# Kernel tuning notes

Hardware: AMD Instinct MI355X
Metric: run time of the kernel (lower is better)

Reference implementation:

```python
import jax, jax.numpy as jnp
import numpy as np

EPS = 1e-6  # torch F.pairwise_distance default eps added to the difference


def setup_inputs() -> dict:
    key = jax.random.key(0)
    k1, k2 = jax.random.split(key)
    x = jax.random.normal(k1, (8, 4096, 512), dtype=jnp.float32)
    centroids = jax.random.normal(k2, (2048, 512), dtype=jnp.float32)
    return {"x": x, "centroids": centroids}


def reference(x, centroids):
    # Faithful to KMeans.forward with normalize=None, p_norm=2, return_centroids=True.
    # torch pairwise_distance computes ||x - c + eps||_2; expand algebraically with
    # xe = x + eps to avoid materializing the (b, k, d) broadcast:
    #   ||xe - c||^2 = ||xe||^2 - 2 xe.c + ||c||^2
    batch_shape = x.shape[:-1]
    d = x.shape[-1]
    xf = x.reshape(-1, d)                    # (b, d)
    xe = xf + EPS
    x_sq = jnp.sum(xe * xe, axis=-1, keepdims=True)          # (b, 1)
    c_sq = jnp.sum(centroids * centroids, axis=-1)[None, :]  # (1, k)
    sq = x_sq + c_sq - 2.0 * (xe @ centroids.T)              # (b, k)
    dist = jnp.sqrt(jnp.maximum(sq, 0.0))
    labels = jnp.argmin(dist, axis=-1)                        # (b,)
    assigned = centroids[labels]                              # (b, d)
    labels = labels.reshape(batch_shape)
    assigned = assigned.reshape(*batch_shape, d)
    return labels, assigned
```

## Files before the change

kernel.cpp:

```cpp
#include <hip/hip_runtime.h>
#include <hip/hip_bf16.h>


#define EPS 1e-6f
#define TAU 0.3f

constexpr int BROWS = 32768;
constexpr int DD    = 512;
constexpr int KC    = 2048;
constexpr int FCAP  = 4096;
constexpr int NK    = DD / 32;

typedef _Float16 half8  __attribute__((ext_vector_type(8)));
typedef _Float16 half4v __attribute__((ext_vector_type(4)));
typedef float    f32x4  __attribute__((ext_vector_type(4)));

__global__ __launch_bounds__(256) void prep_x(const float* __restrict__ x,
                                              _Float16* __restrict__ xh) {
    size_t i = ((size_t)blockIdx.x * 256 + threadIdx.x) * 4;
    float4 v = *(const float4*)(x + i);
    half4v h;
    h[0] = (_Float16)(v.x + EPS); h[1] = (_Float16)(v.y + EPS);
    h[2] = (_Float16)(v.z + EPS); h[3] = (_Float16)(v.w + EPS);
    *(half4v*)(xh + i) = h;
}

__global__ __launch_bounds__(256) void prep_c(const float* __restrict__ cen,
                                              _Float16* __restrict__ ch,
                                              float* __restrict__ csq) {
    int w = threadIdx.x >> 6, lane = threadIdx.x & 63;
    int c = blockIdx.x * 4 + w;
    const float* row = cen + (size_t)c * DD;
    float4 v0 = *(const float4*)(row + lane * 8);
    float4 v1 = *(const float4*)(row + lane * 8 + 4);
    half8 h;
    h[0] = (_Float16)v0.x; h[1] = (_Float16)v0.y; h[2] = (_Float16)v0.z; h[3] = (_Float16)v0.w;
    h[4] = (_Float16)v1.x; h[5] = (_Float16)v1.y; h[6] = (_Float16)v1.z; h[7] = (_Float16)v1.w;
    *(half8*)(ch + (size_t)c * DD + lane * 8) = h;
    float s = v0.x*v0.x + v0.y*v0.y + v0.z*v0.z + v0.w*v0.w
            + v1.x*v1.x + v1.y*v1.y + v1.z*v1.z + v1.w*v1.w;
    #pragma unroll
    for (int off = 32; off > 0; off >>= 1) s += __shfl_down(s, off, 64);
    if (lane == 0) csq[c] = s;
}

__global__ __launch_bounds__(256, 4) void dist_f16(const _Float16* __restrict__ xh,
                                                   const _Float16* __restrict__ ch,
                                                   const float* __restrict__ csq,
                                                   float* __restrict__ pbest,
                                                   float* __restrict__ psec,
                                                   int*   __restrict__ pidx) {
    __shared__ __align__(16) _Float16 smem[5 * 4096];

    const int tid = threadIdx.x;
    const int w = tid >> 6, lane = tid & 63;
    const int wr = w >> 1, wc = w & 1;
    const int quad = lane >> 4, u = lane & 15;
    const int rowBase = blockIdx.x * 128;
    const int colBase = blockIdx.y * 128;

    float cq[4];
    #pragma unroll
    for (int fc = 0; fc < 4; fc++) cq[fc] = csq[colBase + wc * 64 + fc * 16 + u];

    const int g0 = 128 * w + lane;
    const int g1 = g0 + 64;
    const int r0 = g0 >> 2, h0 = g0 & 3;
    const int r1 = g1 >> 2, h1 = g1 & 3;
    const _Float16* pa0 = xh + (size_t)(rowBase + r0) * DD + h0 * 8;
    const _Float16* pa1 = xh + (size_t)(rowBase + r1) * DD + h1 * 8;
    const _Float16* pb0 = ch + (size_t)(colBase + r0) * DD + h0 * 8;
    const _Float16* pb1 = ch + (size_t)(colBase + r1) * DD + h1 * 8;

    auto stageA = [&](int kt) {
        _Float16* dst = smem + (kt % 3) * 4096;
        const int off = kt * 32;
        __builtin_amdgcn_global_load_lds(
            (const __attribute__((address_space(1))) void*)(pa0 + off),
            (__attribute__((address_space(3))) void*)(dst + g0 * 8), 16, 0, 0);
        __builtin_amdgcn_global_load_lds(
            (const __attribute__((address_space(1))) void*)(pa1 + off),
            (__attribute__((address_space(3))) void*)(dst + g1 * 8), 16, 0, 0);
    };
    auto stageB = [&](int kt) {
        _Float16* dst = smem + 12288 + (kt % 2) * 4096;
        const int off = kt * 32;
        __builtin_amdgcn_global_load_lds(
            (const __attribute__((address_space(1))) void*)(pb0 + off),
            (__attribute__((address_space(3))) void*)(dst + g0 * 8), 16, 0, 0);
        __builtin_amdgcn_global_load_lds(
            (const __attribute__((address_space(1))) void*)(pb1 + off),
            (__attribute__((address_space(3))) void*)(dst + g1 * 8), 16, 0, 0);
    };

    f32x4 acc[4][4] = {};

    stageA(0); stageB(0); stageA(1);

    #pragma unroll
    for (int kc = 0; kc < NK; kc++) {
        if (kc + 1 < NK) asm volatile("s_waitcnt vmcnt(2)" ::: "memory");
        else             asm volatile("s_waitcnt vmcnt(0)" ::: "memory");
        __builtin_amdgcn_s_barrier();
        asm volatile("" ::: "memory");
        __builtin_amdgcn_sched_barrier(0);

        if (kc + 1 < NK) stageB(kc + 1);
        if (kc + 2 < NK) stageA(kc + 2);

        const _Float16* abuf = smem + (kc % 3) * 4096;
        const _Float16* bbuf = smem + 12288 + (kc % 2) * 4096;
        half8 af[4], bf[4];
        #pragma unroll
        for (int f = 0; f < 4; f++) {
            af[f] = *(const half8*)(abuf + (wr * 64 + f * 16 + u) * 32 + quad * 8);
            bf[f] = *(const half8*)(bbuf + (wc * 64 + f * 16 + u) * 32 + quad * 8);
        }
        #pragma unroll
        for (int fr = 0; fr < 4; fr++)
            #pragma unroll
            for (int fc = 0; fc < 4; fc++)
                acc[fr][fc] = __builtin_amdgcn_mfma_f32_16x16x32_f16(af[fr], bf[fc], acc[fr][fc], 0, 0, 0);
    }

    __syncthreads();

    float* ebf = (float*)smem;
    float* esf = ebf + 256;
    int*   eif = (int*)(esf + 256);

    const int cbi = blockIdx.y * 2 + wc;
    const int colQuadBase = colBase + wc * 64;

    #pragma unroll
    for (int fr = 0; fr < 4; fr++) {
        #pragma unroll
        for (int reg = 0; reg < 4; reg++) {
            float vv[4];
            #pragma unroll
            for (int fc = 0; fc < 4; fc++) vv[fc] = cq[fc] - 2.0f * acc[fr][fc][reg];
            float mn01 = fminf(vv[0], vv[1]), mx01 = fmaxf(vv[0], vv[1]);
            float mn23 = fminf(vv[2], vv[3]), mx23 = fmaxf(vv[2], vv[3]);
            float b = fminf(mn01, mn23);
            float s = fminf(fmaxf(mn01, mn23), fminf(mx01, mx23));
            #pragma unroll
            for (int m = 1; m < 16; m <<= 1) {
                float ob = __shfl_xor(b, m, 64);
                float os = __shfl_xor(s, m, 64);
                s = fminf(fminf(s, os), fmaxf(b, ob));
                b = fminf(b, ob);
            }
            int bi = 0x7fffffff;
            #pragma unroll
            for (int fc = 0; fc < 4; fc++) {
                unsigned long long mm = __ballot(vv[fc] == b);
                unsigned q16 = (unsigned)((mm >> (quad * 16)) & 0xFFFFu);
                if (bi == 0x7fffffff && q16)
                    bi = colQuadBase + fc * 16 + (__ffs(q16) - 1);
            }
            if (u == 0) {
                int rl = fr * 16 + quad * 4 + reg;
                ebf[w * 64 + rl] = b; esf[w * 64 + rl] = s; eif[w * 64 + rl] = bi;
            }
        }
    }
    __syncthreads();
    {
        const int base = cbi * BROWS + rowBase + wr * 64;
        pbest[base + lane] = ebf[w * 64 + lane];
        psec [base + lane] = esf[w * 64 + lane];
        pidx [base + lane] = eif[w * 64 + lane];
    }
}

__global__ __launch_bounds__(256) void reduce_rows(const float* __restrict__ pbest,
                                                   const float* __restrict__ psec,
                                                   const int* __restrict__ pidx,
                                                   float* __restrict__ out,
                                                   int* __restrict__ labels,
                                                   int* __restrict__ rlist,
                                                   int* __restrict__ ctr) {
    int row = blockIdx.x * 256 + threadIdx.x;
    float b = 3.4e38f, s = 3.4e38f; int bi = 0x7fffffff;
    for (int p = 0; p < 32; p++) {
        float v  = pbest[p * BROWS + row];
        float sv = psec [p * BROWS + row];
        int   vi = pidx [p * BROWS + row];
        if (v < b) { s = fminf(b, fminf(s, sv)); b = v; bi = vi; }
        else       { s = fminf(s, fminf(v, sv)); }
    }
    out[row] = (float)bi;
    labels[row] = bi;
    if (s - b < TAU) {
        int slot = atomicAdd(ctr, 1);
        if (slot < FCAP) rlist[slot] = row;
    }
}

__global__ __launch_bounds__(256, 2) void fixup_dist(const float* __restrict__ x,
                                                     const float* __restrict__ cen,
                                                     const float* __restrict__ csq,
                                                     const int* __restrict__ rlist,
                                                     const int* __restrict__ ctr,
                                                     float* __restrict__ fbest,
                                                     int*   __restrict__ fidx) {
    int n = min(*ctr, FCAP);
    int tilebase = blockIdx.y * 128;
    if (tilebase >= n) return;

    __shared__ float xs[16][132];
    __shared__ float cs[16][132];
    __shared__ float redv[128][17];
    __shared__ int   redi[128][17];
    __shared__ int   rows[128];

    const int tid = threadIdx.x;
    if (tid < 128) rows[tid] = rlist[tilebase + tid];
    __syncthreads();

    const int ty = tid >> 4, tx = tid & 15;
    const int colBase = blockIdx.x * 128;

    float acc[8][8] = {};
    for (int dk = 0; dk < DD; dk += 16) {
        #pragma unroll
        for (int sI = 0; sI < 2; sI++) {
            int id = tid + sI * 256;
            int r  = id >> 2;
            int dc = (id & 3) * 4;
            float4 xv = *(const float4*)(x + (size_t)rows[r] * DD + dk + dc);
            xs[dc + 0][r] = xv.x + EPS; xs[dc + 1][r] = xv.y + EPS;
            xs[dc + 2][r] = xv.z + EPS; xs[dc + 3][r] = xv.w + EPS;
            float4 cv = *(const float4*)(cen + (size_t)(colBase + r) * DD + dk + dc);
            cs[dc + 0][r] = cv.x; cs[dc + 1][r] = cv.y;
            cs[dc + 2][r] = cv.z; cs[dc + 3][r] = cv.w;
        }
        __syncthreads();
        #pragma unroll
        for (int k = 0; k < 16; k++) {
            float4 a0 = *(const float4*)&xs[k][ty * 4];
            float4 a1 = *(const float4*)&xs[k][64 + ty * 4];
            float4 b0 = *(const float4*)&cs[k][tx * 4];
            float4 b1 = *(const float4*)&cs[k][64 + tx * 4];
            float a[8] = {a0.x, a0.y, a0.z, a0.w, a1.x, a1.y, a1.z, a1.w};
            float b[8] = {b0.x, b0.y, b0.z, b0.w, b1.x, b1.y, b1.z, b1.w};
            #pragma unroll
            for (int i = 0; i < 8; i++)
                #pragma unroll
                for (int j = 0; j < 8; j++)
                    acc[i][j] += a[i] * b[j];
        }
        __syncthreads();
    }

    float bv[8]; int bix[8];
    #pragma unroll
    for (int i = 0; i < 8; i++) { bv[i] = 3.4e38f; bix[i] = 0x7fffffff; }
    #pragma unroll
    for (int j = 0; j < 8; j++) {
        int col = colBase + ((j < 4) ? (tx * 4 + j) : (64 + tx * 4 + (j - 4)));
        float cq = csq[col];
        #pragma unroll
        for (int i = 0; i < 8; i++) {
            float v = cq - 2.0f * acc[i][j];
            if (v < bv[i] || (v == bv[i] && col < bix[i])) { bv[i] = v; bix[i] = col; }
        }
    }
    #pragma unroll
    for (int i = 0; i < 8; i++) {
        int r = (i < 4) ? (ty * 4 + i) : (64 + ty * 4 + (i - 4));
        redv[r][tx] = bv[i]; redi[r][tx] = bix[i];
    }
    __syncthreads();
    if (tid < 128) {
        float b = 3.4e38f; int bi = 0x7fffffff;
        #pragma unroll
        for (int t = 0; t < 16; t++) {
            float v = redv[tid][t]; int ix = redi[tid][t];
            if (v < b || (v == b && ix < bi)) { b = v; bi = ix; }
        }
        fbest[blockIdx.x * FCAP + tilebase + tid] = b;
        fidx [blockIdx.x * FCAP + tilebase + tid] = bi;
    }
}

__global__ __launch_bounds__(256) void fixup_reduce(const float* __restrict__ fbest,
                                                    const int* __restrict__ fidx,
                                                    const int* __restrict__ rlist,
                                                    const int* __restrict__ ctr,
                                                    float* __restrict__ out,
                                                    int* __restrict__ labels) {
    int s = blockIdx.x * 256 + threadIdx.x;
    int n = min(*ctr, FCAP);
    if (s >= n) return;
    float b = 3.4e38f; int bi = 0x7fffffff;
    for (int c = 0; c < 16; c++) {
        float v = fbest[c * FCAP + s]; int ix = fidx[c * FCAP + s];
        if (v < b || (v == b && ix < bi)) { b = v; bi = ix; }
    }
    int row = rlist[s];
    out[row] = (float)bi;
    labels[row] = bi;
}

__global__ __launch_bounds__(256) void gather(const float* __restrict__ cen,
                                              const int* __restrict__ labels,
                                              float* __restrict__ out) {
    __shared__ int lab[8];
    const int tid = threadIdx.x;
    const int rowBase = blockIdx.x * 8;
    if (tid < 8) lab[tid] = labels[rowBase + tid];
    __syncthreads();
    float* assigned = out + BROWS;
    #pragma unroll 4
    for (int s = tid; s < 8 * 128; s += 256) {
        int r = s >> 7;
        int f = (s & 127) * 4;
        float4 v = *(const float4*)(cen + (size_t)lab[r] * DD + f);
        *(float4*)(assigned + (size_t)(rowBase + r) * DD + f) = v;
    }
}

extern "C" void kernel_launch(void* const* d_in, const int* in_sizes, int n_in,
                              void* d_out, int out_size, void* d_ws, size_t ws_size,
                              hipStream_t stream) {
    const float* x   = (const float*)d_in[0];
    const float* cen = (const float*)d_in[1];

    char* base = (char*)d_ws;
    _Float16* xh   = (_Float16*)(base);
    _Float16* ch   = (_Float16*)(base + 33554432);
    float* csq     = (float*)(base + 35651584);
    float* pbest   = (float*)(base + 35659776);
    float* psec    = (float*)(base + 39854080);
    int*   pidx    = (int*)  (base + 44048384);
    int*   labels  = (int*)  (base + 48242688);
    int*   rlist   = (int*)  (base + 48373760);
    float* fbest   = (float*)(base + 48390144);
    int*   fidx    = (int*)  (base + 48652288);
    int*   ctr     = (int*)  (base + 48914432);

    hipMemsetAsync(ctr, 0, 4, stream);
    hipMemsetAsync(rlist, 0, FCAP * 4, stream);

    prep_x<<<BROWS * DD / 4 / 256, 256, 0, stream>>>(x, xh);
    prep_c<<<KC / 4, 256, 0, stream>>>(cen, ch, csq);
    dist_f16<<<dim3(BROWS / 128, KC / 128), 256, 0, stream>>>(xh, ch, csq, pbest, psec, pidx);
    reduce_rows<<<BROWS / 256, 256, 0, stream>>>(pbest, psec, pidx, (float*)d_out, labels, rlist, ctr);
    fixup_dist<<<dim3(KC / 128, FCAP / 128), 256, 0, stream>>>(x, cen, csq, rlist, ctr, fbest, fidx);
    fixup_reduce<<<FCAP / 256, 256, 0, stream>>>(fbest, fidx, rlist, ctr, (float*)d_out, labels);
    gather<<<BROWS / 8, 256, 0, stream>>>(cen, labels, (float*)d_out);
}
```

Measured before the change: 311.7 us.

## Enlarge distance GEMM tile to 256x256 with 8 waves and fuse prep kernels

The f16 MFMA distance kernel moves from 128x128 tiles with 4 waves to 256x256 tiles with 8 waves, each wave accumulating a 128x64 sub-tile. This doubles operand reuse from LDS and halves global traffic per output. The x and centroid prep kernels are merged into one launch that also zeroes the counter, and the two memsets are dropped; fixup_dist now guards reads of the row list instead of relying on a zeroed buffer. The cost is much higher register pressure (128 accumulator floats per lane under launch_bounds(512,2)), which risks spills or lower occupancy. The main k-loop is also no longer fully unrolled.

Result: slower. 318.8 us (+2.3%).

```diff
diff --git a/kernel.cpp b/kernel.cpp
--- a/kernel.cpp
+++ b/kernel.cpp
@@ -15,49 +15,53 @@
 typedef _Float16 half4v __attribute__((ext_vector_type(4)));
 typedef float    f32x4  __attribute__((ext_vector_type(4)));
 
-__global__ __launch_bounds__(256) void prep_x(const float* __restrict__ x,
-                                              _Float16* __restrict__ xh) {
-    size_t i = ((size_t)blockIdx.x * 256 + threadIdx.x) * 4;
-    float4 v = *(const float4*)(x + i);
-    half4v h;
-    h[0] = (_Float16)(v.x + EPS); h[1] = (_Float16)(v.y + EPS);
-    h[2] = (_Float16)(v.z + EPS); h[3] = (_Float16)(v.w + EPS);
-    *(half4v*)(xh + i) = h;
-}
-
-__global__ __launch_bounds__(256) void prep_c(const float* __restrict__ cen,
-                                              _Float16* __restrict__ ch,
-                                              float* __restrict__ csq) {
-    int w = threadIdx.x >> 6, lane = threadIdx.x & 63;
-    int c = blockIdx.x * 4 + w;
-    const float* row = cen + (size_t)c * DD;
-    float4 v0 = *(const float4*)(row + lane * 8);
-    float4 v1 = *(const float4*)(row + lane * 8 + 4);
-    half8 h;
-    h[0] = (_Float16)v0.x; h[1] = (_Float16)v0.y; h[2] = (_Float16)v0.z; h[3] = (_Float16)v0.w;
-    h[4] = (_Float16)v1.x; h[5] = (_Float16)v1.y; h[6] = (_Float16)v1.z; h[7] = (_Float16)v1.w;
-    *(half8*)(ch + (size_t)c * DD + lane * 8) = h;
-    float s = v0.x*v0.x + v0.y*v0.y + v0.z*v0.z + v0.w*v0.w
-            + v1.x*v1.x + v1.y*v1.y + v1.z*v1.z + v1.w*v1.w;
-    #pragma unroll
-    for (int off = 32; off > 0; off >>= 1) s += __shfl_down(s, off, 64);
-    if (lane == 0) csq[c] = s;
-}
-
-__global__ __launch_bounds__(256, 4) void dist_f16(const _Float16* __restrict__ xh,
+__global__ __launch_bounds__(256) void prep(const float* __restrict__ x,
+                                            const float* __restrict__ cen,
+                                            _Float16* __restrict__ xh,
+                                            _Float16* __restrict__ ch,
+                                            float* __restrict__ csq,
+                                            int* __restrict__ ctr) {
+    const int bid = blockIdx.x;
+    if (bid < KC / 4) {
+        if (bid == 0 && threadIdx.x == 0) *ctr = 0;
+        int w = threadIdx.x >> 6, lane = threadIdx.x & 63;
+        int c = bid * 4 + w;
+        const float* row = cen + (size_t)c * DD;
+        float4 v0 = *(const float4*)(row + lane * 8);
+        float4 v1 = *(const float4*)(row + lane * 8 + 4);
+        half8 h;
+        h[0] = (_Float16)v0.x; h[1] = (_Float16)v0.y; h[2] = (_Float16)v0.z; h[3] = (_Float16)v0.w;
+        h[4] = (_Float16)v1.x; h[5] = (_Float16)v1.y; h[6] = (_Float16)v1.z; h[7] = (_Float16)v1.w;
+        *(half8*)(ch + (size_t)c * DD + lane * 8) = h;
+        float s = v0.x*v0.x + v0.y*v0.y + v0.z*v0.z + v0.w*v0.w
+                + v1.x*v1.x + v1.y*v1.y + v1.z*v1.z + v1.w*v1.w;
+        #pragma unroll
+        for (int off = 32; off > 0; off >>= 1) s += __shfl_down(s, off, 64);
+        if (lane == 0) csq[c] = s;
+    } else {
+        size_t i = ((size_t)(bid - KC / 4) * 256 + threadIdx.x) * 4;
+        float4 v = *(const float4*)(x + i);
+        half4v h;
+        h[0] = (_Float16)(v.x + EPS); h[1] = (_Float16)(v.y + EPS);
+        h[2] = (_Float16)(v.z + EPS); h[3] = (_Float16)(v.w + EPS);
+        *(half4v*)(xh + i) = h;
+    }
+}
+
+__global__ __launch_bounds__(512, 2) void dist_f16(const _Float16* __restrict__ xh,
                                                    const _Float16* __restrict__ ch,
                                                    const float* __restrict__ csq,
                                                    float* __restrict__ pbest,
                                                    float* __restrict__ psec,
                                                    int*   __restrict__ pidx) {
-    __shared__ __align__(16) _Float16 smem[5 * 4096];
+    __shared__ __align__(16) _Float16 smem[5 * 8192];
 
     const int tid = threadIdx.x;
     const int w = tid >> 6, lane = tid & 63;
-    const int wr = w >> 1, wc = w & 1;
+    const int wr = w >> 2, wc = w & 3;
     const int quad = lane >> 4, u = lane & 15;
-    const int rowBase = blockIdx.x * 128;
-    const int colBase = blockIdx.y * 128;
+    const int rowBase = blockIdx.x * 256;
+    const int colBase = blockIdx.y * 256;
 
     float cq[4];
     #pragma unroll
@@ -73,7 +77,7 @@
     const _Float16* pb1 = ch + (size_t)(colBase + r1) * DD + h1 * 8;
 
     auto stageA = [&](int kt) {
-        _Float16* dst = smem + (kt % 3) * 4096;
+        _Float16* dst = smem + (kt % 3) * 8192;
         const int off = kt * 32;
         __builtin_amdgcn_global_load_lds(
             (const __attribute__((address_space(1))) void*)(pa0 + off),
@@ -83,7 +87,7 @@
             (__attribute__((address_space(3))) void*)(dst + g1 * 8), 16, 0, 0);
     };
     auto stageB = [&](int kt) {
-        _Float16* dst = smem + 12288 + (kt % 2) * 4096;
+        _Float16* dst = smem + 24576 + (kt % 2) * 8192;
         const int off = kt * 32;
         __builtin_amdgcn_global_load_lds(
             (const __attribute__((address_space(1))) void*)(pb0 + off),
@@ -93,11 +97,10 @@
             (__attribute__((address_space(3))) void*)(dst + g1 * 8), 16, 0, 0);
     };
 
-    f32x4 acc[4][4] = {};
+    f32x4 acc[8][4] = {};
 
     stageA(0); stageB(0); stageA(1);
 
-    #pragma unroll
     for (int kc = 0; kc < NK; kc++) {
         if (kc + 1 < NK) asm volatile("s_waitcnt vmcnt(2)" ::: "memory");
         else             asm volatile("s_waitcnt vmcnt(0)" ::: "memory");
@@ -108,16 +111,18 @@
         if (kc + 1 < NK) stageB(kc + 1);
         if (kc + 2 < NK) stageA(kc + 2);
 
-        const _Float16* abuf = smem + (kc % 3) * 4096;
-        const _Float16* bbuf = smem + 12288 + (kc % 2) * 4096;
-        half8 af[4], bf[4];
-        #pragma unroll
-        for (int f = 0; f < 4; f++) {
-            af[f] = *(const half8*)(abuf + (wr * 64 + f * 16 + u) * 32 + quad * 8);
+        const _Float16* abuf = smem + (kc % 3) * 8192;
+        const _Float16* bbuf = smem + 24576 + (kc % 2) * 8192;
+        half8 af[8], bf[4];
+        #pragma unroll
+        for (int f = 0; f < 8; f++)
+            af[f] = *(const half8*)(abuf + (wr * 128 + f * 16 + u) * 32 + quad * 8);
+        #pragma unroll
+        for (int f = 0; f < 4; f++)
             bf[f] = *(const half8*)(bbuf + (wc * 64 + f * 16 + u) * 32 + quad * 8);
-        }
-        #pragma unroll
-        for (int fr = 0; fr < 4; fr++)
+
+        #pragma unroll
+        for (int fr = 0; fr < 8; fr++)
             #pragma unroll
             for (int fc = 0; fc < 4; fc++)
                 acc[fr][fc] = __builtin_amdgcn_mfma_f32_16x16x32_f16(af[fr], bf[fc], acc[fr][fc], 0, 0, 0);
@@ -126,14 +131,14 @@
     __syncthreads();
 
     float* ebf = (float*)smem;
-    float* esf = ebf + 256;
-    int*   eif = (int*)(esf + 256);
-
-    const int cbi = blockIdx.y * 2 + wc;
+    float* esf = ebf + 8 * 128;
+    int*   eif = (int*)(esf + 8 * 128);
+
+    const int cbi = blockIdx.y * 4 + wc;
     const int colQuadBase = colBase + wc * 64;
 
     #pragma unroll
-    for (int fr = 0; fr < 4; fr++) {
+    for (int fr = 0; fr < 8; fr++) {
         #pragma unroll
         for (int reg = 0; reg < 4; reg++) {
             float vv[4];
@@ -160,16 +165,19 @@
             }
             if (u == 0) {
                 int rl = fr * 16 + quad * 4 + reg;
-                ebf[w * 64 + rl] = b; esf[w * 64 + rl] = s; eif[w * 64 + rl] = bi;
+                ebf[w * 128 + rl] = b; esf[w * 128 + rl] = s; eif[w * 128 + rl] = bi;
             }
         }
     }
     __syncthreads();
     {
-        const int base = cbi * BROWS + rowBase + wr * 64;
-        pbest[base + lane] = ebf[w * 64 + lane];
-        psec [base + lane] = esf[w * 64 + lane];
-        pidx [base + lane] = eif[w * 64 + lane];
+        const int base = cbi * BROWS + rowBase + wr * 128;
+        pbest[base + lane]      = ebf[w * 128 + lane];
+        pbest[base + 64 + lane] = ebf[w * 128 + 64 + lane];
+        psec [base + lane]      = esf[w * 128 + lane];
+        psec [base + 64 + lane] = esf[w * 128 + 64 + lane];
+        pidx [base + lane]      = eif[w * 128 + lane];
+        pidx [base + 64 + lane] = eif[w * 128 + 64 + lane];
     }
 }
 
@@ -215,7 +223,10 @@
     __shared__ int   rows[128];
 
     const int tid = threadIdx.x;
-    if (tid < 128) rows[tid] = rlist[tilebase + tid];
+    if (tid < 128) {
+        int ii = tilebase + tid;
+        rows[tid] = (ii < n) ? rlist[ii] : 0;
+    }
     __syncthreads();
 
     const int ty = tid >> 4, tx = tid & 15;
@@ -340,12 +351,8 @@
     int*   fidx    = (int*)  (base + 48652288);
     int*   ctr     = (int*)  (base + 48914432);
 
-    hipMemsetAsync(ctr, 0, 4, stream);
-    hipMemsetAsync(rlist, 0, FCAP * 4, stream);
-
-    prep_x<<<BROWS * DD / 4 / 256, 256, 0, stream>>>(x, xh);
-    prep_c<<<KC / 4, 256, 0, stream>>>(cen, ch, csq);
-    dist_f16<<<dim3(BROWS / 128, KC / 128), 256, 0, stream>>>(xh, ch, csq, pbest, psec, pidx);
+    prep<<<KC / 4 + BROWS * DD / 4 / 256, 256, 0, stream>>>(x, cen, xh, ch, csq, ctr);
+    dist_f16<<<dim3(BROWS / 256, KC / 256), 512, 0, stream>>>(xh, ch, csq, pbest, psec, pidx);
     reduce_rows<<<BROWS / 256, 256, 0, stream>>>(pbest, psec, pidx, (float*)d_out, labels, rlist, ctr);
     fixup_dist<<<dim3(KC / 128, FCAP / 128), 256, 0, stream>>>(x, cen, csq, rlist, ctr, fbest, fidx);
     fixup_reduce<<<FCAP / 256, 256, 0, stream>>>(fbest, fidx, rlist, ctr, (float*)d_out, labels);
```

## Rewrite fixup GEMM with split-f16 MFMA, async LDS loads, and fused prep

Applied to the files above, without the earlier changes.

The fp32 fixup distance kernel, which uses scalar FMAs over 16-wide k-chunks, is replaced by an MFMA version. It splits fp32 operands into hi/lo f16 pairs (three products), stages tiles with double-buffered global_load_lds and an XOR swizzle, and reduces argmin with wave shuffles. The prep_x and prep_c kernels are merged into one launch that also zeroes the counter, removing two memsets and one launch. The split-f16 trick gives only near-fp32 accuracy, so near-tie rows could resolve differently. Padded rows now read rlist[0] rather than relying on the zeroed list.

Measured after the change: 274.4 us. 12.0% less time.

```diff
diff --git a/kernel.cpp b/kernel.cpp
--- a/kernel.cpp
+++ b/kernel.cpp
@@ -15,33 +15,37 @@
 typedef _Float16 half4v __attribute__((ext_vector_type(4)));
 typedef float    f32x4  __attribute__((ext_vector_type(4)));
 
-__global__ __launch_bounds__(256) void prep_x(const float* __restrict__ x,
-                                              _Float16* __restrict__ xh) {
-    size_t i = ((size_t)blockIdx.x * 256 + threadIdx.x) * 4;
-    float4 v = *(const float4*)(x + i);
-    half4v h;
-    h[0] = (_Float16)(v.x + EPS); h[1] = (_Float16)(v.y + EPS);
-    h[2] = (_Float16)(v.z + EPS); h[3] = (_Float16)(v.w + EPS);
-    *(half4v*)(xh + i) = h;
-}
-
-__global__ __launch_bounds__(256) void prep_c(const float* __restrict__ cen,
-                                              _Float16* __restrict__ ch,
-                                              float* __restrict__ csq) {
-    int w = threadIdx.x >> 6, lane = threadIdx.x & 63;
-    int c = blockIdx.x * 4 + w;
-    const float* row = cen + (size_t)c * DD;
-    float4 v0 = *(const float4*)(row + lane * 8);
-    float4 v1 = *(const float4*)(row + lane * 8 + 4);
-    half8 h;
-    h[0] = (_Float16)v0.x; h[1] = (_Float16)v0.y; h[2] = (_Float16)v0.z; h[3] = (_Float16)v0.w;
-    h[4] = (_Float16)v1.x; h[5] = (_Float16)v1.y; h[6] = (_Float16)v1.z; h[7] = (_Float16)v1.w;
-    *(half8*)(ch + (size_t)c * DD + lane * 8) = h;
-    float s = v0.x*v0.x + v0.y*v0.y + v0.z*v0.z + v0.w*v0.w
-            + v1.x*v1.x + v1.y*v1.y + v1.z*v1.z + v1.w*v1.w;
-    #pragma unroll
-    for (int off = 32; off > 0; off >>= 1) s += __shfl_down(s, off, 64);
-    if (lane == 0) csq[c] = s;
+__global__ __launch_bounds__(256) void prep(const float* __restrict__ x,
+                                            const float* __restrict__ cen,
+                                            _Float16* __restrict__ xh,
+                                            _Float16* __restrict__ ch,
+                                            float* __restrict__ csq,
+                                            int* __restrict__ ctr) {
+    const int bid = blockIdx.x;
+    if (bid < KC / 4) {
+        if (bid == 0 && threadIdx.x == 0) *ctr = 0;
+        int w = threadIdx.x >> 6, lane = threadIdx.x & 63;
+        int c = bid * 4 + w;
+        const float* row = cen + (size_t)c * DD;
+        float4 v0 = *(const float4*)(row + lane * 8);
+        float4 v1 = *(const float4*)(row + lane * 8 + 4);
+        half8 h;
+        h[0] = (_Float16)v0.x; h[1] = (_Float16)v0.y; h[2] = (_Float16)v0.z; h[3] = (_Float16)v0.w;
+        h[4] = (_Float16)v1.x; h[5] = (_Float16)v1.y; h[6] = (_Float16)v1.z; h[7] = (_Float16)v1.w;
+        *(half8*)(ch + (size_t)c * DD + lane * 8) = h;
+        float s = v0.x*v0.x + v0.y*v0.y + v0.z*v0.z + v0.w*v0.w
+                + v1.x*v1.x + v1.y*v1.y + v1.z*v1.z + v1.w*v1.w;
+        #pragma unroll
+        for (int off = 32; off > 0; off >>= 1) s += __shfl_down(s, off, 64);
+        if (lane == 0) csq[c] = s;
+    } else {
+        size_t i = ((size_t)(bid - KC / 4) * 256 + threadIdx.x) * 4;
+        float4 v = *(const float4*)(x + i);
+        half4v h;
+        h[0] = (_Float16)(v.x + EPS); h[1] = (_Float16)(v.y + EPS);
+        h[2] = (_Float16)(v.z + EPS); h[3] = (_Float16)(v.w + EPS);
+        *(half4v*)(xh + i) = h;
+    }
 }
 
 __global__ __launch_bounds__(256, 4) void dist_f16(const _Float16* __restrict__ xh,
@@ -208,77 +212,140 @@
     int tilebase = blockIdx.y * 128;
     if (tilebase >= n) return;
 
-    __shared__ float xs[16][132];
-    __shared__ float cs[16][132];
-    __shared__ float redv[128][17];
-    __shared__ int   redi[128][17];
-    __shared__ int   rows[128];
+    __shared__ __align__(16) float asmem[2][128 * 32];
+    __shared__ __align__(16) float bsmem[2][128 * 32];
+    __shared__ int   rows_s[128];
+    __shared__ float fb[2][128];
+    __shared__ int   fi[2][128];
 
     const int tid = threadIdx.x;
-    if (tid < 128) rows[tid] = rlist[tilebase + tid];
+    if (tid < 128) {
+        int ii = tilebase + tid;
+        rows_s[tid] = (ii < n) ? rlist[ii] : rlist[0];
+    }
     __syncthreads();
 
-    const int ty = tid >> 4, tx = tid & 15;
+    const int w = tid >> 6, lane = tid & 63;
+    const int wr = w >> 1, wc = w & 1;
+    const int quad = lane >> 4, u = lane & 15;
     const int colBase = blockIdx.x * 128;
 
-    float acc[8][8] = {};
-    for (int dk = 0; dk < DD; dk += 16) {
-        #pragma unroll
-        for (int sI = 0; sI < 2; sI++) {
-            int id = tid + sI * 256;
-            int r  = id >> 2;
-            int dc = (id & 3) * 4;
-            float4 xv = *(const float4*)(x + (size_t)rows[r] * DD + dk + dc);
-            xs[dc + 0][r] = xv.x + EPS; xs[dc + 1][r] = xv.y + EPS;
-            xs[dc + 2][r] = xv.z + EPS; xs[dc + 3][r] = xv.w + EPS;
-            float4 cv = *(const float4*)(cen + (size_t)(colBase + r) * DD + dk + dc);
-            cs[dc + 0][r] = cv.x; cs[dc + 1][r] = cv.y;
-            cs[dc + 2][r] = cv.z; cs[dc + 3][r] = cv.w;
+    const float* pa[4]; const float* pb[4]; int ldsg[4];
+    #pragma unroll
+    for (int j = 0; j < 4; j++) {
+        int g = j * 256 + tid;
+        int r = g >> 3, s = (g & 7) ^ (r & 7);
+        pa[j] = x   + (size_t)rows_s[r] * DD + s * 4;
+        pb[j] = cen + (size_t)(colBase + r) * DD + s * 4;
+        ldsg[j] = g * 4;
+    }
+
+    auto stage = [&](int kt) {
+        float* da = asmem[kt & 1];
+        float* db = bsmem[kt & 1];
+        const int off = kt * 32;
+        #pragma unroll
+        for (int j = 0; j < 4; j++) {
+            __builtin_amdgcn_global_load_lds(
+                (const __attribute__((address_space(1))) void*)(pa[j] + off),
+                (__attribute__((address_space(3))) void*)(da + ldsg[j]), 16, 0, 0);
+            __builtin_amdgcn_global_load_lds(
+                (const __attribute__((address_space(1))) void*)(pb[j] + off),
+                (__attribute__((address_space(3))) void*)(db + ldsg[j]), 16, 0, 0);
         }
-        __syncthreads();
-        #pragma unroll
-        for (int k = 0; k < 16; k++) {
-            float4 a0 = *(const float4*)&xs[k][ty * 4];
-            float4 a1 = *(const float4*)&xs[k][64 + ty * 4];
-            float4 b0 = *(const float4*)&cs[k][tx * 4];
-            float4 b1 = *(const float4*)&cs[k][64 + tx * 4];
-            float a[8] = {a0.x, a0.y, a0.z, a0.w, a1.x, a1.y, a1.z, a1.w};
-            float b[8] = {b0.x, b0.y, b0.z, b0.w, b1.x, b1.y, b1.z, b1.w};
-            #pragma unroll
-            for (int i = 0; i < 8; i++)
+    };
+
+    f32x4 acc[4][4] = {};
+    stage(0);
+
+    for (int kc = 0; kc < NK; kc++) {
+        asm volatile("s_waitcnt vmcnt(0)" ::: "memory");
+        __builtin_amdgcn_s_barrier();
+        asm volatile("" ::: "memory");
+        __builtin_amdgcn_sched_barrier(0);
+        if (kc + 1 < NK) stage(kc + 1);
+
+        const float* ab = asmem[kc & 1];
+        const float* bb = bsmem[kc & 1];
+        half8 aH[4], aL[4], bH[4], bL[4];
+        #pragma unroll
+        for (int f = 0; f < 4; f++) {
+            {
+                const float* base = ab + (wr * 64 + f * 16 + u) * 32;
+                int s0 = ((quad << 1) | 0) ^ (u & 7);
+                int s1 = ((quad << 1) | 1) ^ (u & 7);
+                float4 v0 = *(const float4*)(base + s0 * 4);
+                float4 v1 = *(const float4*)(base + s1 * 4);
+                float fs[8] = {v0.x, v0.y, v0.z, v0.w, v1.x, v1.y, v1.z, v1.w};
                 #pragma unroll
-                for (int j = 0; j < 8; j++)
-                    acc[i][j] += a[i] * b[j];
+                for (int e = 0; e < 8; e++) {
+                    float fe = fs[e] + EPS;
+                    _Float16 hi = (_Float16)fe;
+                    aH[f][e] = hi;
+                    aL[f][e] = (_Float16)(fe - (float)hi);
+                }
+            }
+            {
+                const float* base = bb + (wc * 64 + f * 16 + u) * 32;
+                int s0 = ((quad << 1) | 0) ^ (u & 7);
+                int s1 = ((quad << 1) | 1) ^ (u & 7);
+                float4 v0 = *(const float4*)(base + s0 * 4);
+                float4 v1 = *(const float4*)(base + s1 * 4);
+                float fs[8] = {v0.x, v0.y, v0.z, v0.w, v1.x, v1.y, v1.z, v1.w};
+                #pragma unroll
+                for (int e = 0; e < 8; e++) {
+                    float fe = fs[e];
+                    _Float16 hi = (_Float16)fe;
+                    bH[f][e] = hi;
+                    bL[f][e] = (_Float16)(fe - (float)hi);
+                }
+            }
         }
-        __syncthreads();
-    }
-
-    float bv[8]; int bix[8];
-    #pragma unroll
-    for (int i = 0; i < 8; i++) { bv[i] = 3.4e38f; bix[i] = 0x7fffffff; }
-    #pragma unroll
-    for (int j = 0; j < 8; j++) {
-        int col = colBase + ((j < 4) ? (tx * 4 + j) : (64 + tx * 4 + (j - 4)));
-        float cq = csq[col];
-        #pragma unroll
-        for (int i = 0; i < 8; i++) {
-            float v = cq - 2.0f * acc[i][j];
-            if (v < bv[i] || (v == bv[i] && col < bix[i])) { bv[i] = v; bix[i] = col; }
+        #pragma unroll
+        for (int fr = 0; fr < 4; fr++)
+            #pragma unroll
+            for (int fc = 0; fc < 4; fc++) {
+                acc[fr][fc] = __builtin_amdgcn_mfma_f32_16x16x32_f16(aH[fr], bL[fc], acc[fr][fc], 0, 0, 0);
+                acc[fr][fc] = __builtin_amdgcn_mfma_f32_16x16x32_f16(aL[fr], bH[fc], acc[fr][fc], 0, 0, 0);
+                acc[fr][fc] = __builtin_amdgcn_mfma_f32_16x16x32_f16(aH[fr], bH[fc], acc[fr][fc], 0, 0, 0);
+            }
+    }
+
+    float cqv[4];
+    #pragma unroll
+    for (int fc = 0; fc < 4; fc++) cqv[fc] = csq[colBase + wc * 64 + fc * 16 + u];
+    const int colQuadBase = colBase + wc * 64;
+
+    #pragma unroll
+    for (int fr = 0; fr < 4; fr++) {
+        #pragma unroll
+        for (int reg = 0; reg < 4; reg++) {
+            float b = 3.4e38f; int bi = 0x7fffffff;
+            #pragma unroll
+            for (int fc = 0; fc < 4; fc++) {
+                float v = cqv[fc] - 2.0f * acc[fr][fc][reg];
+                int c = colQuadBase + fc * 16 + u;
+                if (v < b || (v == b && c < bi)) { b = v; bi = c; }
+            }
+            #pragma unroll
+            for (int m = 1; m < 16; m <<= 1) {
+                float ob = __shfl_xor(b, m, 64);
+                int  obi = __shfl_xor(bi, m, 64);
+                if (ob < b || (ob == b && obi < bi)) { b = ob; bi = obi; }
+            }
+            if (u == 0) {
+                int rl = wr * 64 + fr * 16 + quad * 4 + reg;
+                fb[wc][rl] = b; fi[wc][rl] = bi;
+            }
         }
-    }
-    #pragma unroll
-    for (int i = 0; i < 8; i++) {
-        int r = (i < 4) ? (ty * 4 + i) : (64 + ty * 4 + (i - 4));
-        redv[r][tx] = bv[i]; redi[r][tx] = bix[i];
     }
     __syncthreads();
     if (tid < 128) {
-        float b = 3.4e38f; int bi = 0x7fffffff;
-        #pragma unroll
-        for (int t = 0; t < 16; t++) {
-            float v = redv[tid][t]; int ix = redi[tid][t];
-            if (v < b || (v == b && ix < bi)) { b = v; bi = ix; }
-        }
+        float b0 = fb[0][tid]; int i0 = fi[0][tid];
+        float b1 = fb[1][tid]; int i1 = fi[1][tid];
+        float b; int bi;
+        if (b1 < b0 || (b1 == b0 && i1 < i0)) { b = b1; bi = i1; }
+        else                                  { b = b0; bi = i0; }
         fbest[blockIdx.x * FCAP + tilebase + tid] = b;
         fidx [blockIdx.x * FCAP + tilebase + tid] = bi;
     }
@@ -340,11 +407,7 @@
     int*   fidx    = (int*)  (base + 48652288);
     int*   ctr     = (int*)  (base + 48914432);
 
-    hipMemsetAsync(ctr, 0, 4, stream);
-    hipMemsetAsync(rlist, 0, FCAP * 4, stream);
-
-    prep_x<<<BROWS * DD / 4 / 256, 256, 0, stream>>>(x, xh);
-    prep_c<<<KC / 4, 256, 0, stream>>>(cen, ch, csq);
+    prep<<<KC / 4 + BROWS * DD / 4 / 256, 256, 0, stream>>>(x, cen, xh, ch, csq, ctr);
     dist_f16<<<dim3(BROWS / 128, KC / 128), 256, 0, stream>>>(xh, ch, csq, pbest, psec, pidx);
     reduce_rows<<<BROWS / 256, 256, 0, stream>>>(pbest, psec, pidx, (float*)d_out, labels, rlist, ctr);
     fixup_dist<<<dim3(KC / 128, FCAP / 128), 256, 0, stream>>>(x, cen, csq, rlist, ctr, fbest, fidx);
```
